# Optimization experiments

Measured on AMD Instinct MI355X. Metric: run time of the kernel, lower is better.

Reference implementation:

```python
import jax, jax.numpy as jnp
import numpy as np

N_CAT = (50, 50, 50, 50)
N_SAMPLES = 8_000_000


def setup_inputs() -> dict:
    key = jax.random.key(0)
    k1, k2 = jax.random.split(key)
    probs = jax.random.uniform(k1, N_CAT, dtype=jnp.float32)
    probs = probs / probs.sum()  # valid joint probability table
    X = jax.random.randint(k2, (N_SAMPLES, len(N_CAT)), 0, 50, dtype=jnp.int64)
    return {"probs": probs, "X": X}


def reference(probs, X):
    # Faithful to log_probability: out[i] = probs[tuple(X[i])]
    # Vectorized as a ravel-multi-index + single flat gather.
    shape = probs.shape
    strides = jnp.array(
        [int(np.prod(shape[i + 1:], dtype=np.int64)) for i in range(len(shape))],
        dtype=X.dtype,
    )  # [d]
    flat_idx = (X * strides).sum(axis=1)  # [N]
    return probs.reshape(-1)[flat_idx]  # [N]
```

## Files before the change

kernel.cpp:

```cpp
#include <hip/hip_runtime.h>
#include <hip/hip_bf16.h>

__global__ __launch_bounds__(256) void jc_gather_kernel(
    const int4* __restrict__ X,
    const float* __restrict__ probs,
    float* __restrict__ out,
    int n)
{
    int i = blockIdx.x * blockDim.x + threadIdx.x;
    if (i < n) {
        int4 x = X[i];
        int idx = x.x * 125000 + x.y * 2500 + x.z * 50 + x.w;
        out[i] = probs[idx];
    }
}

extern "C" void kernel_launch(void* const* d_in, const int* in_sizes, int n_in,
                              void* d_out, int out_size, void* d_ws, size_t ws_size,
                              hipStream_t stream) {
    const float* probs = (const float*)d_in[0];
    const int4*  X     = (const int4*)d_in[1];
    float* out = (float*)d_out;

    int n = out_size;
    int block = 256;
    int grid = (n + block - 1) / block;
    jc_gather_kernel<<<grid, block, 0, stream>>>(X, probs, out, n);
}
```

Before: 289.5 us.

## Partition gather table across XCCs so each die's L2 serves one slice

Splits the work into an index-computing kernel that writes flat indices to workspace, then a persistent gather kernel where each XCC (read via hardware register) scans every index but only services those falling in its own eighth of the 25 MB table. The aim is to keep each XCC's working set of the probability table small enough to stay resident in its local L2 and cut random DRAM/MALL traffic. In exchange, every XCC rereads the full index array (8x index reads), adds an extra pass plus a memset and launch, and relies on dynamic atomic chunking. It also assumes exactly 8 XCCs and that blocks exist on every XCC, otherwise some outputs are never written.

Measured after the change: 469.0 us. 62.0% more time.

```diff
diff --git a/kernel.cpp b/kernel.cpp
--- a/kernel.cpp
+++ b/kernel.cpp
@@ -1,17 +1,76 @@
 #include <hip/hip_runtime.h>
 #include <hip/hip_bf16.h>
 
-__global__ __launch_bounds__(256) void jc_gather_kernel(
-    const int4* __restrict__ X,
-    const float* __restrict__ probs,
-    float* __restrict__ out,
-    int n)
-{
+
+typedef int v4i __attribute__((ext_vector_type(4)));
+
+#define TABLE_SIZE 6250000
+#define N_SLICES   8
+#define SLICE_SZ   ((TABLE_SIZE + N_SLICES - 1) / N_SLICES)
+#define CHUNK      4096
+
+__device__ __forceinline__ int get_xcc_id() {
+    int x;
+    asm volatile("s_getreg_b32 %0, hwreg(HW_REG_XCC_ID)" : "=s"(x));
+    return x & 7;
+}
+
+__global__ __launch_bounds__(256) void k_index(const v4i* __restrict__ X,
+                                               int* __restrict__ idx, int n) {
     int i = blockIdx.x * blockDim.x + threadIdx.x;
     if (i < n) {
-        int4 x = X[i];
-        int idx = x.x * 125000 + x.y * 2500 + x.z * 50 + x.w;
-        out[i] = probs[idx];
+        v4i x = __builtin_nontemporal_load(&X[i]);
+        int id = x.x * 125000 + x.y * 2500 + x.z * 50 + x.w;
+        __builtin_nontemporal_store(id, &idx[i]);
+    }
+}
+
+__global__ __launch_bounds__(256) void k_gather(const int* __restrict__ idx,
+                                                const float* __restrict__ probs,
+                                                float* __restrict__ out,
+                                                int* __restrict__ counters, int n) {
+    const int xcc = get_xcc_id();
+    const int lo = xcc * SLICE_SZ;
+    const int hi = lo + SLICE_SZ;
+    const v4i* idx4 = (const v4i*)idx;
+    __shared__ int s_c;
+
+    for (;;) {
+        if (threadIdx.x == 0) s_c = atomicAdd(&counters[xcc], CHUNK);
+        __syncthreads();
+        int c = s_c;
+        __syncthreads();
+        if (c >= n) break;
+
+        #pragma unroll
+        for (int k = 0; k < CHUNK / (256 * 4); ++k) {
+            int i0 = c + (threadIdx.x + k * 256) * 4;
+            if (i0 + 3 < n) {
+                v4i v = __builtin_nontemporal_load(&idx4[i0 >> 2]);
+                if (v.x >= lo && v.x < hi) __builtin_nontemporal_store(probs[v.x], &out[i0]);
+                if (v.y >= lo && v.y < hi) __builtin_nontemporal_store(probs[v.y], &out[i0 + 1]);
+                if (v.z >= lo && v.z < hi) __builtin_nontemporal_store(probs[v.z], &out[i0 + 2]);
+                if (v.w >= lo && v.w < hi) __builtin_nontemporal_store(probs[v.w], &out[i0 + 3]);
+            } else {
+                for (int m = 0; m < 4; ++m) {
+                    int i = i0 + m;
+                    if (i < n) {
+                        int v = idx[i];
+                        if (v >= lo && v < hi) __builtin_nontemporal_store(probs[v], &out[i]);
+                    }
+                }
+            }
+        }
+    }
+}
+
+__global__ __launch_bounds__(256) void k_simple(const v4i* __restrict__ X,
+                                                const float* __restrict__ probs,
+                                                float* __restrict__ out, int n) {
+    int i = blockIdx.x * blockDim.x + threadIdx.x;
+    if (i < n) {
+        v4i x = X[i];
+        out[i] = probs[x.x * 125000 + x.y * 2500 + x.z * 50 + x.w];
     }
 }
 
@@ -19,11 +78,23 @@
                               void* d_out, int out_size, void* d_ws, size_t ws_size,
                               hipStream_t stream) {
     const float* probs = (const float*)d_in[0];
-    const int4*  X     = (const int4*)d_in[1];
+    const v4i*   X     = (const v4i*)d_in[1];
     float* out = (float*)d_out;
+    int n = out_size;
 
-    int n = out_size;
+    size_t need = 256 + (size_t)n * sizeof(int);
+    if (ws_size < need) {
+        int block = 256;
+        k_simple<<<(n + block - 1) / block, block, 0, stream>>>(X, probs, out, n);
+        return;
+    }
+
+    int* counters = (int*)d_ws;
+    int* idx      = (int*)((char*)d_ws + 256);
+
+    hipMemsetAsync(counters, 0, 256, stream);
+
     int block = 256;
-    int grid = (n + block - 1) / block;
-    jc_gather_kernel<<<grid, block, 0, stream>>>(X, probs, out, n);
+    k_index<<<(n + block - 1) / block, block, 0, stream>>>(X, idx, n);
+    k_gather<<<2048, block, 0, stream>>>(idx, probs, out, counters, n);
 }
```
